# Optimization experiments

Hardware: AMD Instinct MI355X
Metric: run time of the kernel (lower is better)

## Reference

```python
import jax, jax.numpy as jnp
import numpy as np

B, S, IN, H = 16, 512, 512, 256
TAU_TRACE = 20.0
TAU_MEM = 20.0
DECAY_TRACE = float(np.exp(-1.0 / TAU_TRACE))  # exp_convolve decay
DECAY_MEM = float(np.exp(-1.0 / TAU_MEM))      # leaky-integrator dynamics decay
LR = 0.01                                       # plasticity learning rate
W_MAX = 1.0                                     # soft upper bound on fast weights


def setup_inputs() -> dict:
    key = jax.random.key(0)
    k1, k2 = jax.random.split(key)
    x = jax.random.normal(k1, (B, S, IN), dtype=jnp.float32)
    # xavier_uniform with gain=sqrt(2) on W of shape [2H, IN]
    lim = float(np.sqrt(2.0) * np.sqrt(6.0 / (2 * H + IN)))
    W = jax.random.uniform(k2, (2 * H, IN), dtype=jnp.float32, minval=-lim, maxval=lim)
    return {"x": x, "W": W}


def reference(x, W):
    # i = x @ W^T : [B, S, 2H], then split into key/value input currents
    i = jnp.einsum('bsi,hi->bsh', x, W)
    ik, iv = jnp.split(i, 2, axis=2)  # each [B, S, H]
    bsz = x.shape[0]
    h = W.shape[0] // 2

    def step(carry, inp):
        kv, vv, kt, vt, mem = carry
        ik_t, iv_t = inp  # [B, H] each
        # key dynamics (leaky integrator + tanh)
        kv = DECAY_MEM * kv + ik_t
        key = jnp.tanh(kv)
        # memory readout: 0.2 * (key.unsqueeze(1) * mem).sum(2) == 0.2 * mem @ key
        ikv = 0.2 * jnp.einsum('bij,bj->bi', mem, key)
        # value dynamics
        vv = DECAY_MEM * vv + iv_t + ikv
        val = jnp.tanh(vv)
        # exponential traces
        kt = DECAY_TRACE * kt + (1.0 - DECAY_TRACE) * key
        vt = DECAY_TRACE * vt + (1.0 - DECAY_TRACE) * val
        # soft-bounded Hebbian outer-product fast-weight update
        mem = mem + LR * (vt[:, :, None] * kt[:, None, :]) * (W_MAX - mem)
        return (kv, vv, kt, vt, mem), (key, val)

    z = jnp.zeros((bsz, h), x.dtype)
    mem0 = jnp.zeros((bsz, h, h), x.dtype)
    (_, _, _, _, mem), (keys, vals) = jax.lax.scan(
        step, (z, z, z, z, mem0),
        (jnp.swapaxes(ik, 0, 1), jnp.swapaxes(iv, 0, 1)))  # scan over time
    return mem, jnp.swapaxes(keys, 0, 1), jnp.swapaxes(vals, 0, 1)
```

## Files before the change

kernel.cpp:

```cpp
#include <hip/hip_runtime.h>

#define BB 16
#define SS 512
#define KIN 512
#define H 256

typedef float v2f __attribute__((ext_vector_type(2)));

constexpr float DECAY = 0.951229424500714f;
constexpr float OMD   = 0.048770575499286f;
constexpr float LR    = 0.01f;

__device__ __forceinline__ float fast_tanh(float x) {
    float e = __expf(2.f * x);
    return 1.f - __fdividef(2.f, e + 1.f);
}

__device__ __forceinline__ v2f pk_mul(v2f a, v2f b) {
    v2f d; asm("v_pk_mul_f32 %0, %1, %2" : "=v"(d) : "v"(a), "v"(b)); return d;
}
__device__ __forceinline__ v2f pk_fma(v2f a, v2f b, v2f c) {
    v2f d; asm("v_pk_fma_f32 %0, %1, %2, %3" : "=v"(d) : "v"(a), "v"(b), "v"(c)); return d;
}

__device__ __forceinline__ void half_sum32(float x, float& s_lo, float& s_hi) {
    int t;
    t = __builtin_amdgcn_update_dpp(0, __float_as_int(x), 0x111, 0xf, 0xf, false);
    x += __int_as_float(t);
    t = __builtin_amdgcn_update_dpp(0, __float_as_int(x), 0x112, 0xf, 0xf, false);
    x += __int_as_float(t);
    t = __builtin_amdgcn_update_dpp(0, __float_as_int(x), 0x114, 0xf, 0xf, false);
    x += __int_as_float(t);
    t = __builtin_amdgcn_update_dpp(0, __float_as_int(x), 0x118, 0xf, 0xf, false);
    x += __int_as_float(t);
    t = __builtin_amdgcn_update_dpp(0, __float_as_int(x), 0x142, 0xa, 0xf, false);
    x += __int_as_float(t);
    s_lo = __int_as_float(__builtin_amdgcn_readlane(__float_as_int(x), 31));
    s_hi = __int_as_float(__builtin_amdgcn_readlane(__float_as_int(x), 63));
}

__global__ __launch_bounds__(256) void gemm_xwT(const float* __restrict__ X,
                                                const float* __restrict__ W,
                                                float* __restrict__ ik_out,
                                                float* __restrict__ iv_t) {
    __shared__ float As[16][68];
    __shared__ float Bs[16][68];
    const int m0 = blockIdx.y * 64;
    const int n0 = blockIdx.x * 64;
    const int tid = threadIdx.x;
    const int r  = tid >> 2;
    const int cg = tid & 3;
    const int tx = tid & 15;
    const int ty = tid >> 4;
    float acc[4][4] = {};
    for (int k0 = 0; k0 < KIN; k0 += 16) {
        float4 av = *(const float4*)&X[(size_t)(m0 + r) * KIN + k0 + cg * 4];
        float4 bv = *(const float4*)&W[(size_t)(n0 + r) * KIN + k0 + cg * 4];
        __syncthreads();
        As[cg*4+0][r] = av.x; As[cg*4+1][r] = av.y; As[cg*4+2][r] = av.z; As[cg*4+3][r] = av.w;
        Bs[cg*4+0][r] = bv.x; Bs[cg*4+1][r] = bv.y; Bs[cg*4+2][r] = bv.z; Bs[cg*4+3][r] = bv.w;
        __syncthreads();
#pragma unroll
        for (int kk = 0; kk < 16; ++kk) {
            float4 a = *(const float4*)&As[kk][ty * 4];
            float4 b = *(const float4*)&Bs[kk][tx * 4];
            float ar[4] = {a.x, a.y, a.z, a.w};
            float br[4] = {b.x, b.y, b.z, b.w};
#pragma unroll
            for (int i = 0; i < 4; ++i)
#pragma unroll
                for (int j = 0; j < 4; ++j) acc[i][j] += ar[i] * br[j];
        }
    }
    if (n0 < 256) {
#pragma unroll
        for (int i = 0; i < 4; ++i) {
            float4 o = make_float4(acc[i][0], acc[i][1], acc[i][2], acc[i][3]);
            *(float4*)&ik_out[(size_t)(m0 + ty * 4 + i) * 256 + n0 + tx * 4] = o;
        }
    } else {
        const int b  = m0 >> 9;
        const int s0 = (m0 & 511) + ty * 4;
#pragma unroll
        for (int j = 0; j < 4; ++j) {
            float4 o = make_float4(acc[0][j], acc[1][j], acc[2][j], acc[3][j]);
            *(float4*)&iv_t[((size_t)b * H + (n0 - 256 + tx * 4 + j)) * SS + s0] = o;
        }
    }
}

__global__ __launch_bounds__(64) void key_scan(const float* __restrict__ ik,
                                               float* __restrict__ keys) {
    const int idx = blockIdx.x * 64 + threadIdx.x;
    const int b   = idx >> 8;
    const int col = idx & 255;
    const float* c  = ik + (size_t)b * SS * 256 + col;
    float* ko = keys + (size_t)b * SS * H + col;
    float kv = 0.f;
    constexpr int D = 32;
    float ib[D];
#pragma unroll
    for (int j = 0; j < D; ++j) ib[j] = c[(size_t)j * 256];
    for (int t = 0; t < SS; t += D) {
#pragma unroll
        for (int j = 0; j < D; ++j) {
            float v = ib[j];
            int tn = t + D + j; if (tn > SS - 1) tn = SS - 1;
            ib[j] = c[(size_t)tn * 256];
            kv = DECAY * kv + v;
            ko[(size_t)(t + j) * H] = fast_tanh(kv);
        }
    }
}

__global__ __launch_bounds__(256) void ksum_kernel(const float* __restrict__ keys,
                                                   float* __restrict__ ksum) {
    const int gwave = (blockIdx.x * 256 + threadIdx.x) >> 6;
    const int lane  = threadIdx.x & 63;
    const int b = gwave >> 9;
    const int t = gwave & 511;
    float4 k = *(const float4*)&keys[((size_t)b * SS + t) * H + lane * 4];
    float s = k.x + k.y + k.z + k.w;
#pragma unroll
    for (int off = 1; off < 64; off <<= 1) s += __shfl_xor(s, off);
    if (lane == 0) ksum[(size_t)b * SS + t] = 0.2f * s;
}

__global__ __launch_bounds__(128) void fold_kernel(const float* __restrict__ ksum,
                                                   float* __restrict__ iv_t) {
    const int b   = blockIdx.x >> 8;
    const int row = blockIdx.x & 255;
    const int t   = threadIdx.x * 4;
    float4 ks = *(const float4*)&ksum[(size_t)b * SS + t];
    float* p = &iv_t[((size_t)b * H + row) * SS + t];
    float4 iv = *(const float4*)p;
    iv.x += ks.x; iv.y += ks.y; iv.z += ks.z; iv.w += ks.w;
    *(float4*)p = iv;
}

__global__ __launch_bounds__(256) void value_scan(const float* __restrict__ keys,
                                                  const float* __restrict__ iv_t,
                                                  float* __restrict__ mem_out,
                                                  float* __restrict__ vals) {
    const int tid  = threadIdx.x;
    const int wave = tid >> 6;
    const int lane = tid & 63;
    const int half = lane >> 5;
    const int sub  = lane & 31;
    const int b    = blockIdx.x & 15;
    const int rg   = blockIdx.x >> 4;
    const int row  = rg * 8 + wave * 2 + half;
    const int so   = sub * 8;

    const float* kp  = keys + (size_t)b * SS * H + so;
    const float* ivp = iv_t + ((size_t)b * H + row) * SS;
    float* vp = vals + (size_t)b * SS * H + row;

    const v2f DEC2 = {DECAY, DECAY};
    const v2f OMD2 = {OMD, OMD};

    v2f u[4]   = {{1.f,1.f},{1.f,1.f},{1.f,1.f},{1.f,1.f}};
    v2f ktr[4] = {{0.f,0.f},{0.f,0.f},{0.f,0.f},{0.f,0.f}};
    float vv = 0.f, vt = 0.f;

    v2f kR[8][4];
#pragma unroll
    for (int j = 0; j < 8; ++j)
#pragma unroll
        for (int q = 0; q < 4; ++q)
            kR[j][q] = *(const v2f*)(kp + (size_t)j * H + q * 2);
    kp += 8 * H;

    float4 ivc0 = *(const float4*)(ivp);
    float4 ivc1 = *(const float4*)(ivp + 4);
    ivp += 8;

#define VS_STEP(J, RELOAD, KOFF)                                               \
    {                                                                          \
        v2f kc0 = kR[J][0], kc1 = kR[J][1], kc2 = kR[J][2], kc3 = kR[J][3];    \
        if (RELOAD) {                                                          \
            kR[J][0] = *(const v2f*)(kp + (KOFF) * H + 0);                     \
            kR[J][1] = *(const v2f*)(kp + (KOFF) * H + 2);                     \
            kR[J][2] = *(const v2f*)(kp + (KOFF) * H + 4);                     \
            kR[J][3] = *(const v2f*)(kp + (KOFF) * H + 6);                     \
        }                                                                      \
        v2f p2 = pk_mul(u[0], kc0);                                            \
        p2 = pk_fma(u[1], kc1, p2);                                            \
        p2 = pk_fma(u[2], kc2, p2);                                            \
        p2 = pk_fma(u[3], kc3, p2);                                            \
        float slo, shi;                                                        \
        half_sum32(p2.x + p2.y, slo, shi);                                     \
        float ps = half ? shi : slo;                                           \
        float civ = (J) < 4 ? ((J)==0?ivc0.x:(J)==1?ivc0.y:(J)==2?ivc0.z:ivc0.w)\
                            : ((J)==4?ivc1.x:(J)==5?ivc1.y:(J)==6?ivc1.z:ivc1.w);\
        vv = DECAY * vv + civ;                                                 \
        vv = __builtin_fmaf(-0.2f, ps, vv);                                    \
        float valv = fast_tanh(vv);                                            \
        vt = DECAY * vt + OMD * valv;                                          \
        if (sub == 0) vp[(size_t)((J) & 3) * H] = valv;                        \
        float an = -LR * vt;                                                   \
        v2f an2 = {an, an};                                                    \
        ktr[0] = pk_fma(DEC2, ktr[0], pk_mul(OMD2, kc0));                      \
        ktr[1] = pk_fma(DEC2, ktr[1], pk_mul(OMD2, kc1));                      \
        ktr[2] = pk_fma(DEC2, ktr[2], pk_mul(OMD2, kc2));                      \
        ktr[3] = pk_fma(DEC2, ktr[3], pk_mul(OMD2, kc3));                      \
        u[0] = pk_fma(pk_mul(an2, ktr[0]), u[0], u[0]);                        \
        u[1] = pk_fma(pk_mul(an2, ktr[1]), u[1], u[1]);                        \
        u[2] = pk_fma(pk_mul(an2, ktr[2]), u[2], u[2]);                        \
        u[3] = pk_fma(pk_mul(an2, ktr[3]), u[3], u[3]);                        \
    }

    for (int t0 = 0; t0 < SS - 8; t0 += 8) {
        float4 ivn0 = *(const float4*)(ivp);
        float4 ivn1 = *(const float4*)(ivp + 4);
        ivp += 8;
        VS_STEP(0, true, 0) VS_STEP(1, true, 1) VS_STEP(2, true, 2) VS_STEP(3, true, 3)
        kp += 4 * H; vp += 4 * H;
        VS_STEP(4, true, 0) VS_STEP(5, true, 1) VS_STEP(6, true, 2) VS_STEP(7, true, 3)
        kp += 4 * H; vp += 4 * H;
        ivc0 = ivn0; ivc1 = ivn1;
    }
    VS_STEP(0, false, 0) VS_STEP(1, false, 0) VS_STEP(2, false, 0) VS_STEP(3, false, 0)
    vp += 4 * H;
    VS_STEP(4, false, 0) VS_STEP(5, false, 0) VS_STEP(6, false, 0) VS_STEP(7, false, 0)
#undef VS_STEP

    float* mo = &mem_out[((size_t)b * H + row) * H + so];
    *(float4*)&mo[0] = make_float4(1.f - u[0].x, 1.f - u[0].y, 1.f - u[1].x, 1.f - u[1].y);
    *(float4*)&mo[4] = make_float4(1.f - u[2].x, 1.f - u[2].y, 1.f - u[3].x, 1.f - u[3].y);
}

extern "C" void kernel_launch(void* const* d_in, const int* in_sizes, int n_in,
                              void* d_out, int out_size, void* d_ws, size_t ws_size,
                              hipStream_t stream) {
    const float* x = (const float*)d_in[0];
    const float* W = (const float*)d_in[1];
    float* out = (float*)d_out;
    float* mem_out = out;
    float* keys = out + (size_t)BB * H * H;
    float* vals = keys + (size_t)BB * SS * H;
    float* ik   = (float*)d_ws;
    float* iv_t = ik + (size_t)BB * SS * 256;
    float* ksum = ik;

    dim3 gb(8, 128);
    gemm_xwT<<<gb, 256, 0, stream>>>(x, W, ik, iv_t);
    key_scan<<<64, 64, 0, stream>>>(ik, keys);
    ksum_kernel<<<2048, 256, 0, stream>>>(keys, ksum);
    fold_kernel<<<4096, 128, 0, stream>>>(ksum, iv_t);
    value_scan<<<512, 256, 0, stream>>>(keys, iv_t, mem_out, vals);
}
```

Measured before the change: 267.8 us.

## Track mem directly in value scan, drop ksum/fold kernels, batch val stores

The value scan now carries mem itself instead of u = 1 - mem. That removes the need to precompute per-step key sums and fold them into iv, so two launches and a full read-modify-write of iv_t go away. The scan is unrolled over 16 steps with iv prefetched 16 ahead. Each lane stashes one value and the lanes store once per 16 steps, replacing a single-lane store every step. In exchange the inner step does extra packed ops per element (computing 1 - mem) and holds more registers.

```diff
diff --git a/kernel.cpp b/kernel.cpp
--- a/kernel.cpp
+++ b/kernel.cpp
@@ -113,31 +113,6 @@
     }
 }
 
-__global__ __launch_bounds__(256) void ksum_kernel(const float* __restrict__ keys,
-                                                   float* __restrict__ ksum) {
-    const int gwave = (blockIdx.x * 256 + threadIdx.x) >> 6;
-    const int lane  = threadIdx.x & 63;
-    const int b = gwave >> 9;
-    const int t = gwave & 511;
-    float4 k = *(const float4*)&keys[((size_t)b * SS + t) * H + lane * 4];
-    float s = k.x + k.y + k.z + k.w;
-#pragma unroll
-    for (int off = 1; off < 64; off <<= 1) s += __shfl_xor(s, off);
-    if (lane == 0) ksum[(size_t)b * SS + t] = 0.2f * s;
-}
-
-__global__ __launch_bounds__(128) void fold_kernel(const float* __restrict__ ksum,
-                                                   float* __restrict__ iv_t) {
-    const int b   = blockIdx.x >> 8;
-    const int row = blockIdx.x & 255;
-    const int t   = threadIdx.x * 4;
-    float4 ks = *(const float4*)&ksum[(size_t)b * SS + t];
-    float* p = &iv_t[((size_t)b * H + row) * SS + t];
-    float4 iv = *(const float4*)p;
-    iv.x += ks.x; iv.y += ks.y; iv.z += ks.z; iv.w += ks.w;
-    *(float4*)p = iv;
-}
-
 __global__ __launch_bounds__(256) void value_scan(const float* __restrict__ keys,
                                                   const float* __restrict__ iv_t,
                                                   float* __restrict__ mem_out,
@@ -154,14 +129,16 @@
 
     const float* kp  = keys + (size_t)b * SS * H + so;
     const float* ivp = iv_t + ((size_t)b * H + row) * SS;
-    float* vp = vals + (size_t)b * SS * H + row;
+    float* vrow = vals + (size_t)b * SS * H + row;
 
     const v2f DEC2 = {DECAY, DECAY};
     const v2f OMD2 = {OMD, OMD};
-
-    v2f u[4]   = {{1.f,1.f},{1.f,1.f},{1.f,1.f},{1.f,1.f}};
-    v2f ktr[4] = {{0.f,0.f},{0.f,0.f},{0.f,0.f},{0.f,0.f}};
-    float vv = 0.f, vt = 0.f;
+    const v2f ONE2 = {1.f, 1.f};
+    const v2f NM12 = {-1.f, -1.f};
+
+    v2f mem2[4] = {{0.f,0.f},{0.f,0.f},{0.f,0.f},{0.f,0.f}};
+    v2f ktr[4]  = {{0.f,0.f},{0.f,0.f},{0.f,0.f},{0.f,0.f}};
+    float vv = 0.f, vt = 0.f, stash = 0.f;
 
     v2f kR[8][4];
 #pragma unroll
@@ -171,63 +148,89 @@
             kR[j][q] = *(const v2f*)(kp + (size_t)j * H + q * 2);
     kp += 8 * H;
 
-    float4 ivc0 = *(const float4*)(ivp);
-    float4 ivc1 = *(const float4*)(ivp + 4);
-    ivp += 8;
+    float4 ivA0 = *(const float4*)(ivp);
+    float4 ivA1 = *(const float4*)(ivp + 4);
+    float4 ivB0 = *(const float4*)(ivp + 8);
+    float4 ivB1 = *(const float4*)(ivp + 12);
+    ivp += 16;
 
 #define VS_STEP(J, RELOAD, KOFF)                                               \
     {                                                                          \
-        v2f kc0 = kR[J][0], kc1 = kR[J][1], kc2 = kR[J][2], kc3 = kR[J][3];    \
+        const int SL = (J) & 7;                                                \
+        v2f kc0 = kR[SL][0], kc1 = kR[SL][1], kc2 = kR[SL][2], kc3 = kR[SL][3];\
         if (RELOAD) {                                                          \
-            kR[J][0] = *(const v2f*)(kp + (KOFF) * H + 0);                     \
-            kR[J][1] = *(const v2f*)(kp + (KOFF) * H + 2);                     \
-            kR[J][2] = *(const v2f*)(kp + (KOFF) * H + 4);                     \
-            kR[J][3] = *(const v2f*)(kp + (KOFF) * H + 6);                     \
+            kR[SL][0] = *(const v2f*)(kp + (KOFF) * H + 0);                    \
+            kR[SL][1] = *(const v2f*)(kp + (KOFF) * H + 2);                    \
+            kR[SL][2] = *(const v2f*)(kp + (KOFF) * H + 4);                    \
+            kR[SL][3] = *(const v2f*)(kp + (KOFF) * H + 6);                    \
         }                                                                      \
-        v2f p2 = pk_mul(u[0], kc0);                                            \
-        p2 = pk_fma(u[1], kc1, p2);                                            \
-        p2 = pk_fma(u[2], kc2, p2);                                            \
-        p2 = pk_fma(u[3], kc3, p2);                                            \
+        v2f p2 = pk_mul(mem2[0], kc0);                                         \
+        p2 = pk_fma(mem2[1], kc1, p2);                                         \
+        p2 = pk_fma(mem2[2], kc2, p2);                                         \
+        p2 = pk_fma(mem2[3], kc3, p2);                                         \
         float slo, shi;                                                        \
         half_sum32(p2.x + p2.y, slo, shi);                                     \
         float ps = half ? shi : slo;                                           \
-        float civ = (J) < 4 ? ((J)==0?ivc0.x:(J)==1?ivc0.y:(J)==2?ivc0.z:ivc0.w)\
-                            : ((J)==4?ivc1.x:(J)==5?ivc1.y:(J)==6?ivc1.z:ivc1.w);\
-        vv = DECAY * vv + civ;                                                 \
-        vv = __builtin_fmaf(-0.2f, ps, vv);                                    \
+        float civ = ivs[J];                                                    \
+        vv = __builtin_fmaf(DECAY, vv, civ);                                   \
+        vv = __builtin_fmaf(0.2f, ps, vv);                                     \
         float valv = fast_tanh(vv);                                            \
-        vt = DECAY * vt + OMD * valv;                                          \
-        if (sub == 0) vp[(size_t)((J) & 3) * H] = valv;                        \
-        float an = -LR * vt;                                                   \
-        v2f an2 = {an, an};                                                    \
+        vt = __builtin_fmaf(DECAY, vt, OMD * valv);                            \
+        if (sub == (J)) stash = valv;                                          \
+        float c = LR * vt;                                                     \
+        v2f c2 = {c, c};                                                       \
         ktr[0] = pk_fma(DEC2, ktr[0], pk_mul(OMD2, kc0));                      \
         ktr[1] = pk_fma(DEC2, ktr[1], pk_mul(OMD2, kc1));                      \
         ktr[2] = pk_fma(DEC2, ktr[2], pk_mul(OMD2, kc2));                      \
         ktr[3] = pk_fma(DEC2, ktr[3], pk_mul(OMD2, kc3));                      \
-        u[0] = pk_fma(pk_mul(an2, ktr[0]), u[0], u[0]);                        \
-        u[1] = pk_fma(pk_mul(an2, ktr[1]), u[1], u[1]);                        \
-        u[2] = pk_fma(pk_mul(an2, ktr[2]), u[2], u[2]);                        \
-        u[3] = pk_fma(pk_mul(an2, ktr[3]), u[3], u[3]);                        \
-    }
-
-    for (int t0 = 0; t0 < SS - 8; t0 += 8) {
-        float4 ivn0 = *(const float4*)(ivp);
-        float4 ivn1 = *(const float4*)(ivp + 4);
-        ivp += 8;
-        VS_STEP(0, true, 0) VS_STEP(1, true, 1) VS_STEP(2, true, 2) VS_STEP(3, true, 3)
-        kp += 4 * H; vp += 4 * H;
-        VS_STEP(4, true, 0) VS_STEP(5, true, 1) VS_STEP(6, true, 2) VS_STEP(7, true, 3)
-        kp += 4 * H; vp += 4 * H;
-        ivc0 = ivn0; ivc1 = ivn1;
-    }
-    VS_STEP(0, false, 0) VS_STEP(1, false, 0) VS_STEP(2, false, 0) VS_STEP(3, false, 0)
-    vp += 4 * H;
-    VS_STEP(4, false, 0) VS_STEP(5, false, 0) VS_STEP(6, false, 0) VS_STEP(7, false, 0)
+        v2f d0 = pk_fma(mem2[0], NM12, ONE2);                                  \
+        v2f d1 = pk_fma(mem2[1], NM12, ONE2);                                  \
+        v2f d2 = pk_fma(mem2[2], NM12, ONE2);                                  \
+        v2f d3 = pk_fma(mem2[3], NM12, ONE2);                                  \
+        mem2[0] = pk_fma(pk_mul(c2, ktr[0]), d0, mem2[0]);                     \
+        mem2[1] = pk_fma(pk_mul(c2, ktr[1]), d1, mem2[1]);                     \
+        mem2[2] = pk_fma(pk_mul(c2, ktr[2]), d2, mem2[2]);                     \
+        mem2[3] = pk_fma(pk_mul(c2, ktr[3]), d3, mem2[3]);                     \
+    }
+
+#define VS_TILE16(RELOAD_A, RELOAD_B)                                          \
+    {                                                                          \
+        float ivs[16] = {ivA0.x, ivA0.y, ivA0.z, ivA0.w,                       \
+                         ivA1.x, ivA1.y, ivA1.z, ivA1.w,                       \
+                         ivB0.x, ivB0.y, ivB0.z, ivB0.w,                       \
+                         ivB1.x, ivB1.y, ivB1.z, ivB1.w};                      \
+        VS_STEP(0, RELOAD_A, 0) VS_STEP(1, RELOAD_A, 1)                        \
+        VS_STEP(2, RELOAD_A, 2) VS_STEP(3, RELOAD_A, 3)                        \
+        if (RELOAD_A) kp += 4 * H;                                             \
+        VS_STEP(4, RELOAD_A, 0) VS_STEP(5, RELOAD_A, 1)                        \
+        VS_STEP(6, RELOAD_A, 2) VS_STEP(7, RELOAD_A, 3)                        \
+        if (RELOAD_A) kp += 4 * H;                                             \
+        VS_STEP(8, RELOAD_B, 0) VS_STEP(9, RELOAD_B, 1)                        \
+        VS_STEP(10, RELOAD_B, 2) VS_STEP(11, RELOAD_B, 3)                      \
+        if (RELOAD_B) kp += 4 * H;                                             \
+        VS_STEP(12, RELOAD_B, 0) VS_STEP(13, RELOAD_B, 1)                      \
+        VS_STEP(14, RELOAD_B, 2) VS_STEP(15, RELOAD_B, 3)                      \
+        if (RELOAD_B) kp += 4 * H;                                             \
+        if (sub < 16) vrow[(size_t)sub * H] = stash;                           \
+        vrow += 16 * H;                                                        \
+    }
+
+    for (int t0 = 0; t0 < SS - 16; t0 += 16) {
+        float4 nA0 = *(const float4*)(ivp);
+        float4 nA1 = *(const float4*)(ivp + 4);
+        float4 nB0 = *(const float4*)(ivp + 8);
+        float4 nB1 = *(const float4*)(ivp + 12);
+        ivp += 16;
+        VS_TILE16(true, true)
+        ivA0 = nA0; ivA1 = nA1; ivB0 = nB0; ivB1 = nB1;
+    }
+    VS_TILE16(true, false)
+#undef VS_TILE16
 #undef VS_STEP
 
     float* mo = &mem_out[((size_t)b * H + row) * H + so];
-    *(float4*)&mo[0] = make_float4(1.f - u[0].x, 1.f - u[0].y, 1.f - u[1].x, 1.f - u[1].y);
-    *(float4*)&mo[4] = make_float4(1.f - u[2].x, 1.f - u[2].y, 1.f - u[3].x, 1.f - u[3].y);
+    *(float4*)&mo[0] = make_float4(mem2[0].x, mem2[0].y, mem2[1].x, mem2[1].y);
+    *(float4*)&mo[4] = make_float4(mem2[2].x, mem2[2].y, mem2[3].x, mem2[3].y);
 }
 
 extern "C" void kernel_launch(void* const* d_in, const int* in_sizes, int n_in,
@@ -241,12 +244,9 @@
     float* vals = keys + (size_t)BB * SS * H;
     float* ik   = (float*)d_ws;
     float* iv_t = ik + (size_t)BB * SS * 256;
-    float* ksum = ik;
 
     dim3 gb(8, 128);
     gemm_xwT<<<gb, 256, 0, stream>>>(x, W, ik, iv_t);
     key_scan<<<64, 64, 0, stream>>>(ik, keys);
-    ksum_kernel<<<2048, 256, 0, stream>>>(keys, ksum);
-    fold_kernel<<<4096, 128, 0, stream>>>(ksum, iv_t);
     value_scan<<<512, 256, 0, stream>>>(keys, iv_t, mem_out, vals);
 }
```

Result: faster. 255.1 us (-4.7%).
